# Performance work log

Measured on AMD Instinct MI355X. Metric: run time of the kernel, lower is better.

## Reference

```python
import jax, jax.numpy as jnp
import numpy as np

B, L, V = 128, 32, 10000
IC, WD, H = 2048, 512, 512  # image_code_dim, word_dim, hidden_size (num_layers=1)
D = WD + IC  # GRU input dim


def setup_inputs() -> dict:
    key = jax.random.key(0)
    ks = jax.random.split(key, 10)
    image_code = jax.random.normal(ks[0], (B, IC), dtype=jnp.float32)
    captions = jax.random.randint(ks[1], (B, L), 0, V)
    cap_lens = jax.random.randint(ks[2], (B,), 2, L + 1)
    cap_lens = cap_lens.at[0].set(L)  # pin max length -> static T = L-1
    # parameters (embed/fc match init_weights uniform(-0.1,0.1); GRU/init_state ~ small random)
    embed_w = jax.random.uniform(ks[3], (V, WD), minval=-0.1, maxval=0.1, dtype=jnp.float32)
    W_ih = jax.random.normal(ks[4], (3 * H, D), dtype=jnp.float32) * 0.02
    W_hh = jax.random.normal(ks[5], (3 * H, H), dtype=jnp.float32) * 0.02
    b_ih = jnp.zeros((3 * H,), dtype=jnp.float32)
    b_hh = jnp.zeros((3 * H,), dtype=jnp.float32)
    fc_w = jax.random.uniform(ks[6], (V, H), minval=-0.1, maxval=0.1, dtype=jnp.float32)
    fc_b = jnp.zeros((V,), dtype=jnp.float32)
    init_w = jax.random.normal(ks[7], (H, IC), dtype=jnp.float32) * 0.02  # num_layers*H x IC
    init_b = jnp.zeros((H,), dtype=jnp.float32)
    return {"image_code": image_code, "captions": captions, "cap_lens": cap_lens,
            "embed_w": embed_w, "W_ih": W_ih, "W_hh": W_hh, "b_ih": b_ih, "b_hh": b_hh,
            "fc_w": fc_w, "fc_b": fc_b, "init_w": init_w, "init_b": init_b}


def _gru_decode(image_code, captions_s, lengths, h0, embed_w, W_ih, W_hh, b_ih, b_hh, fc_w, fc_b):
    T = L - 1
    emb = embed_w[captions_s]                      # (B, L, WD)
    xs = jnp.concatenate([
        jnp.broadcast_to(image_code[None], (T, B, IC)),
        jnp.transpose(emb[:, :T, :], (1, 0, 2)),   # (T, B, WD)
    ], axis=-1)                                    # (T, B, D)

    def step(h, x_t):
        gi = x_t @ W_ih.T + b_ih                   # (B, 3H)
        gh = h @ W_hh.T + b_hh                     # (B, 3H)
        i_r, i_z, i_n = jnp.split(gi, 3, axis=-1)
        h_r, h_z, h_n = jnp.split(gh, 3, axis=-1)
        r = jax.nn.sigmoid(i_r + h_r)
        z = jax.nn.sigmoid(i_z + h_z)
        n = jnp.tanh(i_n + r * h_n)
        h_new = (1.0 - z) * n + z * h
        return h_new, h_new

    _, outs = jax.lax.scan(step, h0, xs)           # (T, B, H)
    preds = jnp.einsum('tbh,vh->tbv', outs, fc_w) + fc_b  # dropout is identity in eval
    mask = jnp.arange(T)[:, None] < lengths[None, :]      # (T, B): only active steps
    preds = jnp.where(mask[:, :, None], preds, 0.0)
    return jnp.transpose(preds, (1, 0, 2))         # (B, T, V)


def reference(image_code, captions, cap_lens, embed_w, W_ih, W_hh, b_ih, b_hh, fc_w, fc_b, init_w, init_b):
    order = jnp.argsort(-cap_lens)                 # descending sort like torch.sort(..., True)
    sorted_lens = cap_lens[order]
    captions_s = captions[order]
    image_code_s = image_code[order]
    h0 = image_code_s @ init_w.T + init_b          # (B, H) (num_layers = 1)
    lengths = sorted_lens - 1
    predictions = _gru_decode(image_code_s, captions_s, lengths, h0,
                              embed_w, W_ih, W_hh, b_ih, b_hh, fc_w, fc_b)
    return predictions, captions_s, lengths, order
```

## Files before the change

kernel.cpp:

```cpp
#include <hip/hip_runtime.h>
#include <math.h>

#define B_   128
#define L_   32
#define T_   31
#define V_   10000
#define IC_  2048
#define WD_  512
#define H_   512
#define D_   2560
#define G3_  1536
#define NPAD_ 10112
#define NPROD_ 64
#define NCONS_ 158
#define NTEAM_ 2
#define SU_PFX0 1
#define SU_GI0  17
#define SU_FCW0 389
#define SU_WHH0 2917
#define SU_N    3301

typedef short short8 __attribute__((ext_vector_type(8)));
typedef float f32x4  __attribute__((ext_vector_type(4)));
typedef unsigned short ushort_t;
typedef unsigned long long ull_t;

__device__ __forceinline__ unsigned short f2bf(float f) {
    unsigned int u = __builtin_bit_cast(unsigned int, f);
    unsigned int r = (u + 0x7FFFu + ((u >> 16) & 1u)) >> 16;
    return (unsigned short)r;
}
__device__ __forceinline__ float bf2f(unsigned short h) {
    unsigned int u = ((unsigned int)h) << 16;
    return __builtin_bit_cast(float, u);
}
__device__ __forceinline__ f32x4 mfma16(short8 a, short8 b, f32x4 c) {
    return __builtin_amdgcn_mfma_f32_16x16x32_bf16(a, b, c, 0, 0, 0);
}

#define WS_ORDER  0
#define WS_LEN    512
#define WS_TOK    1024
#define WS_BAR    16896
#define WS_GIIMG  16960
#define WS_WHH    803392
#define WS_GIWEMB 2376256
#define WS_OUTS   14565952
#define WS_FCW    18760256

template<bool F32>
__device__ __forceinline__ uint4 load_cvt(const void* src, size_t off) {
    if constexpr (!F32) {
        return *(const uint4*)((const unsigned short*)src + off);
    } else {
        const float* p = (const float*)src + off;
        const float4 x = *(const float4*)p;
        const float4 y = *(const float4*)(p + 4);
        union { unsigned short u[8]; uint4 v; } r;
        r.u[0]=f2bf(x.x); r.u[1]=f2bf(x.y); r.u[2]=f2bf(x.z); r.u[3]=f2bf(x.w);
        r.u[4]=f2bf(y.x); r.u[5]=f2bf(y.y); r.u[6]=f2bf(y.z); r.u[7]=f2bf(y.w);
        return r.v;
    }
}

__global__ __launch_bounds__(256) void k_setup(
    const int* __restrict__ captions,
    const int* __restrict__ cap_lens,
    const float* __restrict__ fc_w,
    const float* __restrict__ W_hh,
    const float* __restrict__ image_code,
    const float* __restrict__ W_ih,
    const float* __restrict__ b_ih,
    const float* __restrict__ init_w,
    const float* __restrict__ init_b,
    const float* __restrict__ embed_w,
    ushort_t* __restrict__ fcw_bf,
    ushort_t* __restrict__ whh_bf,
    float* __restrict__ gi_img,
    ushort_t* __restrict__ gi_wemb,
    ushort_t* __restrict__ outs,
    int* __restrict__ order,
    int* __restrict__ len_i,
    int* __restrict__ bar,
    float* __restrict__ out_tail)
{
    __shared__ __align__(16) ushort_t As[128 * 32];
    __shared__ __align__(16) ushort_t Bs[128 * 32];
    __shared__ int s_len[B_];
    __shared__ int s_ord[B_];
    const int bid = blockIdx.x;
    const int tid = threadIdx.x;

    if (bid >= SU_FCW0 && bid < SU_WHH0) {
        const int idx = (bid - SU_FCW0) * 256 + tid;
        const int row = idx >> 6;
        const int ch  = idx & 63;
        union { unsigned short u[8]; uint4 v; } r;
        if (row < V_) {
            const float* p = fc_w + (size_t)row * 512 + ch * 8;
            const float4 x = *(const float4*)p;
            const float4 y = *(const float4*)(p + 4);
            r.u[0]=f2bf(x.x); r.u[1]=f2bf(x.y); r.u[2]=f2bf(x.z); r.u[3]=f2bf(x.w);
            r.u[4]=f2bf(y.x); r.u[5]=f2bf(y.y); r.u[6]=f2bf(y.z); r.u[7]=f2bf(y.w);
        } else {
            r.v = make_uint4(0, 0, 0, 0);
        }
        *(uint4*)&fcw_bf[(size_t)row * 512 + ch * 8] = r.v;
        return;
    }
    if (bid >= SU_WHH0) {
        const int idx = (bid - SU_WHH0) * 256 + tid;
        const size_t o = (size_t)idx * 8;
        const int g = (int)(o / (48 * 512));
        const int rem = (int)(o % (48 * 512));
        const int j = rem >> 9;
        const int k = rem & 511;
        const int srow = (j >> 4) * 512 + g * 16 + (j & 15);
        const float* p = W_hh + (size_t)srow * 512 + k;
        const float4 x = *(const float4*)p;
        const float4 y = *(const float4*)(p + 4);
        union { unsigned short u[8]; uint4 v; } r;
        r.u[0]=f2bf(x.x); r.u[1]=f2bf(x.y); r.u[2]=f2bf(x.z); r.u[3]=f2bf(x.w);
        r.u[4]=f2bf(y.x); r.u[5]=f2bf(y.y); r.u[6]=f2bf(y.z); r.u[7]=f2bf(y.w);
        *(uint4*)&whh_bf[o] = r.v;
        return;
    }

    if (tid < B_) s_len[tid] = cap_lens[tid];
    __syncthreads();
    if (tid < B_) {
        const int myl = s_len[tid];
        int rank = 0;
        for (int k = 0; k < B_; ++k) {
            const int lk = s_len[k];
            if (lk > myl || (lk == myl && k < tid)) rank++;
        }
        s_ord[rank] = tid;
    }
    __syncthreads();

    if (bid == 0) {
        if (tid == 0) *bar = 0;
        if (tid < B_) {
            const int o = s_ord[tid];
            order[tid] = o;
            const int ln = s_len[o] - 1;
            len_i[tid] = ln;
            out_tail[B_ * L_ + tid]      = (float)ln;
            out_tail[B_ * L_ + B_ + tid] = (float)o;
        }
        __syncthreads();
        for (int i = tid; i < B_ * L_; i += 256) {
            const int b = i / L_, l = i % L_;
            out_tail[i] = (float)captions[s_ord[b] * L_ + l];
        }
        return;
    }

    const int w = tid >> 6, lane = tid & 63, quad = lane >> 4, lr = lane & 15;
    const int srow = tid >> 2, ch = tid & 3;
    const int wm = (w & 1) * 64, wn = (w >> 1) * 64;

    f32x4 acc[4][4];
    const f32x4 z4 = {0.f, 0.f, 0.f, 0.f};
#pragma unroll
    for (int i = 0; i < 4; ++i)
#pragma unroll
        for (int j = 0; j < 4; ++j) acc[i][j] = z4;

    if (bid >= SU_GI0) {
        const int ti = bid - SU_GI0;
        const int t = ti / 12, nt = ti - t * 12;
        const int n0 = nt * 128;
        const int ar0 = captions[s_ord[srow]      * L_ + t];
        const int ar1 = captions[s_ord[srow + 64] * L_ + t];
        const int br0 = n0 + srow, br1 = n0 + srow + 64;
        const float* Wt = W_ih + IC_;

        uint4 a0 = load_cvt<true>(embed_w, (size_t)ar0 * WD_ + ch * 8);
        uint4 a1 = load_cvt<true>(embed_w, (size_t)ar1 * WD_ + ch * 8);
        uint4 b0 = load_cvt<true>(Wt, (size_t)br0 * D_ + ch * 8);
        uint4 b1 = load_cvt<true>(Wt, (size_t)br1 * D_ + ch * 8);

        for (int k0 = 0; k0 < WD_; k0 += 32) {
            __syncthreads();
            *(uint4*)&As[(srow)      * 32 + ch * 8] = a0;
            *(uint4*)&As[(srow + 64) * 32 + ch * 8] = a1;
            *(uint4*)&Bs[(srow)      * 32 + ch * 8] = b0;
            *(uint4*)&Bs[(srow + 64) * 32 + ch * 8] = b1;
            __syncthreads();
            short8 af[4], bfr[4];
#pragma unroll
            for (int i = 0; i < 4; ++i) af[i]  = *(const short8*)&As[(wm + i * 16 + lr) * 32 + quad * 8];
#pragma unroll
            for (int j = 0; j < 4; ++j) bfr[j] = *(const short8*)&Bs[(wn + j * 16 + lr) * 32 + quad * 8];
            if (k0 + 32 < WD_) {
                a0 = load_cvt<true>(embed_w, (size_t)ar0 * WD_ + k0 + 32 + ch * 8);
                a1 = load_cvt<true>(embed_w, (size_t)ar1 * WD_ + k0 + 32 + ch * 8);
                b0 = load_cvt<true>(Wt, (size_t)br0 * D_ + k0 + 32 + ch * 8);
                b1 = load_cvt<true>(Wt, (size_t)br1 * D_ + k0 + 32 + ch * 8);
            }
#pragma unroll
            for (int i = 0; i < 4; ++i)
#pragma unroll
                for (int j = 0; j < 4; ++j) acc[i][j] = mfma16(af[i], bfr[j], acc[i][j]);
        }

#pragma unroll
        for (int i = 0; i < 4; ++i)
#pragma unroll
            for (int r = 0; r < 4; ++r) {
                const int m = t * 128 + wm + i * 16 + quad * 4 + r;
#pragma unroll
                for (int j = 0; j < 4; ++j) {
                    const int n = n0 + wn + j * 16 + lr;
                    gi_wemb[(size_t)m * G3_ + n] = f2bf(acc[i][j][r]);
                }
            }
        return;
    }

    const int px = bid - SU_PFX0;
    const bool isH0 = px >= 12;
    const float* Bm = isH0 ? init_w : W_ih;
    const int ldb = isH0 ? IC_ : D_;
    const int n0 = isH0 ? (px - 12) * 128 : px * 128;
    const float* bias = isH0 ? init_b : b_ih;

    const int ar0 = s_ord[srow];
    const int ar1 = s_ord[srow + 64];
    const int br0 = n0 + srow, br1 = n0 + srow + 64;

    uint4 a0 = load_cvt<true>(image_code, (size_t)ar0 * IC_ + ch * 8);
    uint4 a1 = load_cvt<true>(image_code, (size_t)ar1 * IC_ + ch * 8);
    uint4 b0 = load_cvt<true>(Bm, (size_t)br0 * ldb + ch * 8);
    uint4 b1 = load_cvt<true>(Bm, (size_t)br1 * ldb + ch * 8);

    for (int k0 = 0; k0 < IC_; k0 += 32) {
        __syncthreads();
        *(uint4*)&As[(srow)      * 32 + ch * 8] = a0;
        *(uint4*)&As[(srow + 64) * 32 + ch * 8] = a1;
        *(uint4*)&Bs[(srow)      * 32 + ch * 8] = b0;
        *(uint4*)&Bs[(srow + 64) * 32 + ch * 8] = b1;
        __syncthreads();
        short8 af[4], bfr[4];
#pragma unroll
        for (int i = 0; i < 4; ++i) af[i]  = *(const short8*)&As[(wm + i * 16 + lr) * 32 + quad * 8];
#pragma unroll
        for (int j = 0; j < 4; ++j) bfr[j] = *(const short8*)&Bs[(wn + j * 16 + lr) * 32 + quad * 8];
        if (k0 + 32 < IC_) {
            a0 = load_cvt<true>(image_code, (size_t)ar0 * IC_ + k0 + 32 + ch * 8);
            a1 = load_cvt<true>(image_code, (size_t)ar1 * IC_ + k0 + 32 + ch * 8);
            b0 = load_cvt<true>(Bm, (size_t)br0 * ldb + k0 + 32 + ch * 8);
            b1 = load_cvt<true>(Bm, (size_t)br1 * ldb + k0 + 32 + ch * 8);
        }
#pragma unroll
        for (int i = 0; i < 4; ++i)
#pragma unroll
            for (int j = 0; j < 4; ++j) acc[i][j] = mfma16(af[i], bfr[j], acc[i][j]);
    }

#pragma unroll
    for (int i = 0; i < 4; ++i)
#pragma unroll
        for (int r = 0; r < 4; ++r) {
            const int m = wm + i * 16 + quad * 4 + r;
#pragma unroll
            for (int j = 0; j < 4; ++j) {
                const int n = n0 + wn + j * 16 + lr;
                const float v = acc[i][j][r] + bias[n];
                if (isH0) outs[(size_t)m * H_ + n] = f2bf(v);
                else      gi_img[(size_t)m * G3_ + n] = v;
            }
        }
}

#define PBS_STR 520
__global__ __launch_bounds__(256, 1) void k_fused(
    const ushort_t* __restrict__ whh_bf,
    const ushort_t* __restrict__ gi_wemb,
    const float* __restrict__ b_hh,
    ushort_t* __restrict__ outs,
    const ushort_t* __restrict__ fcw_bf,
    const float* __restrict__ fc_b,
    const int* __restrict__ len_i,
    float* __restrict__ out,
    int* __restrict__ sync,
    const float* __restrict__ gi_img)
{
    __shared__ __align__(16) ushort_t sm[43008];
    const int bid = blockIdx.x;
    const int tid = threadIdx.x;
    const int w = tid >> 6, lane = tid & 63, quad = lane >> 4, lr = lane & 15;

    if (bid < NPROD_) {
        __builtin_amdgcn_s_setprio(1);
        const int g = bid & 31;
        const int ih = bid >> 5;
        const bool leader = (bid == (ih << 5));
        ushort_t* Bs = sm;

        const ushort_t* wsrc = whh_bf + (size_t)g * 48 * 512;
        for (int i = tid; i < 48 * 64; i += 256) {
            const int row = i >> 6, c = i & 63;
            *(uint4*)&Bs[row * PBS_STR + c * 8] = *(const uint4*)&wsrc[row * 512 + c * 8];
        }
        const int cg = g * 16 + lr;
        const float bhr = b_hh[cg];
        const float bhz = b_hh[512 + cg];
        const float bhn = b_hh[1024 + cg];
        __syncthreads();

        float gim0[4], gim1[4], gim2[4];
        float hold_reg[4];
        {
            const ushort_t* h0p = outs + (size_t)ih * 64 * 512;
#pragma unroll
            for (int r = 0; r < 4; ++r) {
                const int b = ih * 64 + w * 16 + quad * 4 + r;
                const float* pim = gi_img + (size_t)b * G3_ + cg;
                gim0[r] = pim[0]; gim1[r] = pim[512]; gim2[r] = pim[1024];
                hold_reg[r] = bf2f(h0p[(size_t)(w * 16 + quad * 4 + r) * 512 + cg]);
            }
        }
        ushort_t gi0[4], gi1[4], gi2[4];
#pragma unroll
        for (int r = 0; r < 4; ++r) {
            const int b = ih * 64 + w * 16 + quad * 4 + r;
            const ushort_t* p = gi_wemb + (size_t)b * G3_ + cg;
            gi0[r] = p[0]; gi1[r] = p[512]; gi2[r] = p[1024];
        }

        for (int step = 0; step < T_; ++step) {
            const ushort_t* hsrc = outs + (size_t)step * (128 * 512) + (size_t)ih * 64 * 512;

            uint4 hv[16];
            const ushort_t* hrow = hsrc + (size_t)(w * 16 + lr) * 512 + quad * 8;
#pragma unroll
            for (int kk = 0; kk < 16; ++kk)
                hv[kk] = *(const uint4*)(hrow + kk * 32);

            f32x4 acc[3];
#pragma unroll
            for (int j = 0; j < 3; ++j) acc[j] = (f32x4){0.f, 0.f, 0.f, 0.f};
#pragma unroll
            for (int kk = 0; kk < 16; ++kk) {
                union { uint4 v; short8 s; } cc; cc.v = hv[kk];
                const short8 af = cc.s;
#pragma unroll
                for (int j = 0; j < 3; ++j) {
                    const short8 bf = *(const short8*)&Bs[(j * 16 + lr) * PBS_STR + kk * 32 + quad * 8];
                    acc[j] = mfma16(af, bf, acc[j]);
                }
            }

            ushort_t* hdst = outs + (size_t)(step + 1) * (128 * 512);
#pragma unroll
            for (int r = 0; r < 4; ++r) {
                const int b = ih * 64 + w * 16 + quad * 4 + r;
                const float ir  = bf2f(gi0[r]) + gim0[r] + bhr;
                const float iz  = bf2f(gi1[r]) + gim1[r] + bhz;
                const float in_ = bf2f(gi2[r]) + gim2[r];
                const float hr = acc[0][r];
                const float hz = acc[1][r];
                const float hn = acc[2][r] + bhn;
                const float rg = 1.f / (1.f + __expf(-(ir + hr)));
                const float zg = 1.f / (1.f + __expf(-(iz + hz)));
                const float nn = tanhf(in_ + rg * hn);
                const float hnew = (1.f - zg) * nn + zg * hold_reg[r];
                const unsigned int hb = (unsigned int)f2bf(hnew);
                hold_reg[r] = bf2f((unsigned short)hb);
                const unsigned int pv = (unsigned int)__shfl_xor((int)hb, 1);
                if ((lr & 1) == 0) {
                    const unsigned int word = hb | (pv << 16);
                    __hip_atomic_store((unsigned int*)&hdst[(size_t)b * 512 + cg], word,
                                       __ATOMIC_RELAXED, __HIP_MEMORY_SCOPE_AGENT);
                }
            }

            asm volatile("s_waitcnt vmcnt(0)" ::: "memory");
            __syncthreads();
            const int tgt = step + 1;
            if (tid == 0)
                __hip_atomic_store(&sync[bid * 8], tgt,
                                   __ATOMIC_RELAXED, __HIP_MEMORY_SCOPE_AGENT);

            ushort_t ng0[4], ng1[4], ng2[4];
            if (step + 1 < T_) {
                const size_t gb = (size_t)(step + 1) * 128 * G3_;
#pragma unroll
                for (int r = 0; r < 4; ++r) {
                    const int b = ih * 64 + w * 16 + quad * 4 + r;
                    const ushort_t* p = gi_wemb + gb + (size_t)b * G3_ + cg;
                    ng0[r] = p[0]; ng1[r] = p[512]; ng2[r] = p[1024];
                }
            }
            asm volatile("" ::: "memory");

            if (w == 0 && (step < T_ - 1 || leader)) {
                const int* pf = &sync[(ih * 32 + (lane & 31)) * 8];
                for (;;) {
                    const int v = __hip_atomic_load(pf, __ATOMIC_RELAXED, __HIP_MEMORY_SCOPE_AGENT);
                    if (__all(v >= tgt)) break;
                    __builtin_amdgcn_s_sleep(1);
                }
                if (leader && lane == 0) {
#pragma unroll
                    for (int k = 0; k < 8; ++k)
                        __hip_atomic_store(&sync[768 + k * 16 + ih], tgt,
                                           __ATOMIC_RELAXED, __HIP_MEMORY_SCOPE_AGENT);
                }
            }
            __syncthreads();
            asm volatile("" ::: "memory");

            if (step + 1 < T_) {
#pragma unroll
                for (int r = 0; r < 4; ++r) { gi0[r] = ng0[r]; gi1[r] = ng1[r]; gi2[r] = ng2[r]; }
            }
        }
    } else {
        const int cid = bid - NPROD_;
        const int nb = cid % 79;
        const int team = cid / 79;
        const int n0 = nb * 128;
        ushort_t* As = sm;
        ushort_t* Bs = sm + 4096;
        const int srow = tid >> 2, ch = tid & 3;
        const int wm = (w & 1) * 64, wn = (w >> 1) * 64;
        const ull_t* hready = (const ull_t*)&sync[768 + (cid & 7) * 16];

        float fcb[4];
#pragma unroll
        for (int j = 0; j < 4; ++j) {
            const int n = n0 + wn + j * 16 + lr;
            fcb[j] = (n < V_) ? fc_b[n] : 0.f;
        }

        for (int t = team; t < T_; t += NTEAM_) {
            if (tid == 0) {
                for (;;) {
                    const ull_t hv8 = __hip_atomic_load(hready, __ATOMIC_RELAXED, __HIP_MEMORY_SCOPE_AGENT);
                    const int l0 = (int)(unsigned int)(hv8 & 0xffffffffull);
                    const int l1 = (int)(unsigned int)(hv8 >> 32);
                    if (l0 > t && l1 > t) break;
                    __builtin_amdgcn_s_sleep(16);
                }
            }
            __syncthreads();

            const ushort_t* A = outs + (size_t)(t + 1) * (128 * 512);

            f32x4 acc[4][4];
            const f32x4 z4 = {0.f, 0.f, 0.f, 0.f};
#pragma unroll
            for (int i = 0; i < 4; ++i)
#pragma unroll
                for (int j = 0; j < 4; ++j) acc[i][j] = z4;

            uint4 a0 = *(const uint4*)&A[(size_t)srow * 512 + ch * 8];
            uint4 a1 = *(const uint4*)&A[(size_t)(srow + 64) * 512 + ch * 8];
            uint4 b0 = *(const uint4*)&fcw_bf[(size_t)(n0 + srow)      * 512 + ch * 8];
            uint4 b1 = *(const uint4*)&fcw_bf[(size_t)(n0 + srow + 64) * 512 + ch * 8];

            for (int k0 = 0; k0 < 512; k0 += 32) {
                __syncthreads();
                *(uint4*)&As[(srow)      * 32 + ch * 8] = a0;
                *(uint4*)&As[(srow + 64) * 32 + ch * 8] = a1;
                *(uint4*)&Bs[(srow)      * 32 + ch * 8] = b0;
                *(uint4*)&Bs[(srow + 64) * 32 + ch * 8] = b1;
                __syncthreads();
                short8 af[4], bfr[4];
#pragma unroll
                for (int i = 0; i < 4; ++i) af[i]  = *(const short8*)&As[(wm + i * 16 + lr) * 32 + quad * 8];
#pragma unroll
                for (int j = 0; j < 4; ++j) bfr[j] = *(const short8*)&Bs[(wn + j * 16 + lr) * 32 + quad * 8];
                if (k0 + 32 < 512) {
                    a0 = *(const uint4*)&A[(size_t)srow * 512 + k0 + 32 + ch * 8];
                    a1 = *(const uint4*)&A[(size_t)(srow + 64) * 512 + k0 + 32 + ch * 8];
                    b0 = *(const uint4*)&fcw_bf[(size_t)(n0 + srow)      * 512 + k0 + 32 + ch * 8];
                    b1 = *(const uint4*)&fcw_bf[(size_t)(n0 + srow + 64) * 512 + k0 + 32 + ch * 8];
                }
#pragma unroll
                for (int i = 0; i < 4; ++i)
#pragma unroll
                    for (int j = 0; j < 4; ++j) acc[i][j] = mfma16(af[i], bfr[j], acc[i][j]);
            }

#pragma unroll
            for (int i = 0; i < 4; ++i)
#pragma unroll
                for (int r = 0; r < 4; ++r) {
                    const int b = wm + i * 16 + quad * 4 + r;
                    const bool act = (t < len_i[b]);
                    const size_t base = (size_t)b * T_ * V_ + (size_t)t * V_;
#pragma unroll
                    for (int j = 0; j < 4; ++j) {
                        const int n = n0 + wn + j * 16 + lr;
                        if (n < V_) out[base + n] = act ? (acc[i][j][r] + fcb[j]) : 0.f;
                    }
                }
        }
    }
}

extern "C" void kernel_launch(void* const* d_in, const int* in_sizes, int n_in,
                              void* d_out, int out_size, void* d_ws, size_t ws_size,
                              hipStream_t stream) {
    const float* image_code = (const float*)d_in[0];
    const int*   captions   = (const int*)d_in[1];
    const int*   cap_lens   = (const int*)d_in[2];
    const float* embed_w    = (const float*)d_in[3];
    const float* W_ih       = (const float*)d_in[4];
    const float* W_hh       = (const float*)d_in[5];
    const float* b_ih       = (const float*)d_in[6];
    const float* b_hh       = (const float*)d_in[7];
    const float* fc_w       = (const float*)d_in[8];
    const float* fc_b       = (const float*)d_in[9];
    const float* init_w     = (const float*)d_in[10];
    const float* init_b     = (const float*)d_in[11];

    float* out = (float*)d_out;
    char* ws = (char*)d_ws;
    int*      order   = (int*)(ws + WS_ORDER);
    int*      len_i   = (int*)(ws + WS_LEN);
    int*      bar     = (int*)(ws + WS_BAR);
    float*    gi_img  = (float*)(ws + WS_GIIMG);
    ushort_t* whh_bf  = (ushort_t*)(ws + WS_WHH);
    ushort_t* gi_wemb = (ushort_t*)(ws + WS_GIWEMB);
    ushort_t* outs_bf = (ushort_t*)(ws + WS_OUTS);
    ushort_t* fcw_bf  = (ushort_t*)(ws + WS_FCW);
    int*      sync    = (int*)(fcw_bf + ((size_t)NPAD_ - 4) * 512);

    hipLaunchKernelGGL(k_setup, dim3(SU_N), dim3(256), 0, stream,
                       captions, cap_lens, fc_w, W_hh,
                       image_code, W_ih, b_ih, init_w, init_b, embed_w,
                       fcw_bf, whh_bf, gi_img, gi_wemb, outs_bf,
                       order, len_i, bar,
                       out + (size_t)B_ * T_ * V_);

    hipLaunchKernelGGL(k_fused, dim3(NPROD_ + NCONS_), dim3(256), 0, stream,
                       whh_bf, gi_wemb, b_hh, outs_bf,
                       fcw_bf, fc_b, len_i, out, sync, gi_img);
}
```

Measured before the change: 463.4 us.

## Use 1024-thread blocks with 16 producer blocks covering all batch rows

Producer blocks grow to 1024 threads and each now handles two 16-column slices of W_hh across all 128 batch rows, so there are 16 producers instead of 64. The per-step barrier polls fewer flags, and consumers wait on a single ready counter. Consumer blocks also move to 1024 threads, with each warp computing a 32x32 tile and half the threads staging A while the other half stage B. This is meant to cut cross-block synchronisation latency in the recurrent loop, at the cost of more work per producer block and tighter register and occupancy limits with 1024 threads.

```diff
diff --git a/kernel.cpp b/kernel.cpp
--- a/kernel.cpp
+++ b/kernel.cpp
@@ -11,7 +11,7 @@
 #define D_   2560
 #define G3_  1536
 #define NPAD_ 10112
-#define NPROD_ 64
+#define NPROD_ 16
 #define NCONS_ 158
 #define NTEAM_ 2
 #define SU_PFX0 1
@@ -40,7 +40,6 @@
 
 #define WS_ORDER  0
 #define WS_LEN    512
-#define WS_TOK    1024
 #define WS_BAR    16896
 #define WS_GIIMG  16960
 #define WS_WHH    803392
@@ -276,7 +275,7 @@
 }
 
 #define PBS_STR 520
-__global__ __launch_bounds__(256, 1) void k_fused(
+__global__ __launch_bounds__(1024) void k_fused(
     const ushort_t* __restrict__ whh_bf,
     const ushort_t* __restrict__ gi_wemb,
     const float* __restrict__ b_hh,
@@ -288,76 +287,82 @@
     int* __restrict__ sync,
     const float* __restrict__ gi_img)
 {
-    __shared__ __align__(16) ushort_t sm[43008];
+    __shared__ __align__(16) ushort_t sm[2 * 48 * PBS_STR];
     const int bid = blockIdx.x;
     const int tid = threadIdx.x;
     const int w = tid >> 6, lane = tid & 63, quad = lane >> 4, lr = lane & 15;
 
     if (bid < NPROD_) {
         __builtin_amdgcn_s_setprio(1);
-        const int g = bid & 31;
-        const int ih = bid >> 5;
-        const bool leader = (bid == (ih << 5));
+        const int p = bid;
+        const bool leader = (bid == 0);
+        const int slice_sel = w & 1;
+        const int row_grp = w >> 1;
         ushort_t* Bs = sm;
 
-        const ushort_t* wsrc = whh_bf + (size_t)g * 48 * 512;
-        for (int i = tid; i < 48 * 64; i += 256) {
+        for (int i = tid; i < 2 * 48 * 64; i += 1024) {
             const int row = i >> 6, c = i & 63;
-            *(uint4*)&Bs[row * PBS_STR + c * 8] = *(const uint4*)&wsrc[row * 512 + c * 8];
-        }
+            const int s = row >= 48 ? 1 : 0;
+            const int j = row - s * 48;
+            *(uint4*)&Bs[(s * 48 + j) * PBS_STR + c * 8] =
+                *(const uint4*)&whh_bf[((size_t)(2 * p + s) * 48 + j) * 512 + c * 8];
+        }
+        const int g = 2 * p + slice_sel;
         const int cg = g * 16 + lr;
         const float bhr = b_hh[cg];
         const float bhz = b_hh[512 + cg];
         const float bhn = b_hh[1024 + cg];
+        const ushort_t* Bw = Bs + slice_sel * 48 * PBS_STR;
         __syncthreads();
 
         float gim0[4], gim1[4], gim2[4];
         float hold_reg[4];
-        {
-            const ushort_t* h0p = outs + (size_t)ih * 64 * 512;
+#pragma unroll
+        for (int r = 0; r < 4; ++r) {
+            const int b = row_grp * 16 + quad * 4 + r;
+            const float* pim = gi_img + (size_t)b * G3_ + cg;
+            gim0[r] = pim[0]; gim1[r] = pim[512]; gim2[r] = pim[1024];
+            hold_reg[r] = bf2f(outs[(size_t)b * 512 + cg]);
+        }
+        ushort_t gi0[4], gi1[4], gi2[4];
+#pragma unroll
+        for (int r = 0; r < 4; ++r) {
+            const int b = row_grp * 16 + quad * 4 + r;
+            const ushort_t* pg = gi_wemb + (size_t)b * G3_ + cg;
+            gi0[r] = pg[0]; gi1[r] = pg[512]; gi2[r] = pg[1024];
+        }
+
+        for (int step = 0; step < T_; ++step) {
+            const ushort_t* hsrc = outs + (size_t)step * (128 * 512);
+            const ushort_t* hrow = hsrc + (size_t)(row_grp * 16 + lr) * 512 + quad * 8;
+
+            f32x4 acc[3];
+#pragma unroll
+            for (int j = 0; j < 3; ++j) acc[j] = (f32x4){0.f, 0.f, 0.f, 0.f};
+
+#pragma unroll
+            for (int half = 0; half < 2; ++half) {
+                uint4 hv[8];
+#pragma unroll
+                for (int kk = 0; kk < 8; ++kk)
+                    hv[kk] = *(const uint4*)(hrow + (half * 8 + kk) * 32);
+#pragma unroll
+                for (int kk = 0; kk < 8; ++kk) {
+                    union { uint4 v; short8 s; } cc; cc.v = hv[kk];
+                    const short8 af = cc.s;
+                    const int kc = (half * 8 + kk) * 32;
+#pragma unroll
+                    for (int j = 0; j < 3; ++j) {
+                        const short8 bf = *(const short8*)&Bw[(j * 16 + lr) * PBS_STR + kc + quad * 8];
+                        acc[j] = mfma16(af, bf, acc[j]);
+                    }
+                }
+            }
+
+            ushort_t* hdst = outs + (size_t)(step + 1) * (128 * 512);
 #pragma unroll
             for (int r = 0; r < 4; ++r) {
-                const int b = ih * 64 + w * 16 + quad * 4 + r;
-                const float* pim = gi_img + (size_t)b * G3_ + cg;
-                gim0[r] = pim[0]; gim1[r] = pim[512]; gim2[r] = pim[1024];
-                hold_reg[r] = bf2f(h0p[(size_t)(w * 16 + quad * 4 + r) * 512 + cg]);
-            }
-        }
-        ushort_t gi0[4], gi1[4], gi2[4];
-#pragma unroll
-        for (int r = 0; r < 4; ++r) {
-            const int b = ih * 64 + w * 16 + quad * 4 + r;
-            const ushort_t* p = gi_wemb + (size_t)b * G3_ + cg;
-            gi0[r] = p[0]; gi1[r] = p[512]; gi2[r] = p[1024];
-        }
-
-        for (int step = 0; step < T_; ++step) {
-            const ushort_t* hsrc = outs + (size_t)step * (128 * 512) + (size_t)ih * 64 * 512;
-
-            uint4 hv[16];
-            const ushort_t* hrow = hsrc + (size_t)(w * 16 + lr) * 512 + quad * 8;
-#pragma unroll
-            for (int kk = 0; kk < 16; ++kk)
-                hv[kk] = *(const uint4*)(hrow + kk * 32);
-
-            f32x4 acc[3];
-#pragma unroll
-            for (int j = 0; j < 3; ++j) acc[j] = (f32x4){0.f, 0.f, 0.f, 0.f};
-#pragma unroll
-            for (int kk = 0; kk < 16; ++kk) {
-                union { uint4 v; short8 s; } cc; cc.v = hv[kk];
-                const short8 af = cc.s;
-#pragma unroll
-                for (int j = 0; j < 3; ++j) {
-                    const short8 bf = *(const short8*)&Bs[(j * 16 + lr) * PBS_STR + kk * 32 + quad * 8];
-                    acc[j] = mfma16(af, bf, acc[j]);
-                }
-            }
-
-            ushort_t* hdst = outs + (size_t)(step + 1) * (128 * 512);
-#pragma unroll
-            for (int r = 0; r < 4; ++r) {
-                const int b = ih * 64 + w * 16 + quad * 4 + r;
+                const int b = row_grp * 16 + quad * 4 + r;
                 const float ir  = bf2f(gi0[r]) + gim0[r] + bhr;
                 const float iz  = bf2f(gi1[r]) + gim1[r] + bhz;
                 const float in_ = bf2f(gi2[r]) + gim2[r];
@@ -390,15 +395,15 @@
                 const size_t gb = (size_t)(step + 1) * 128 * G3_;
 #pragma unroll
                 for (int r = 0; r < 4; ++r) {
-                    const int b = ih * 64 + w * 16 + quad * 4 + r;
-                    const ushort_t* p = gi_wemb + gb + (size_t)b * G3_ + cg;
-                    ng0[r] = p[0]; ng1[r] = p[512]; ng2[r] = p[1024];
+                    const int b = row_grp * 16 + quad * 4 + r;
+                    const ushort_t* pg = gi_wemb + gb + (size_t)b * G3_ + cg;
+                    ng0[r] = pg[0]; ng1[r] = pg[512]; ng2[r] = pg[1024];
                 }
             }
             asm volatile("" ::: "memory");
 
             if (w == 0 && (step < T_ - 1 || leader)) {
-                const int* pf = &sync[(ih * 32 + (lane & 31)) * 8];
+                const int* pf = &sync[(lane & 15) * 8];
                 for (;;) {
                     const int v = __hip_atomic_load(pf, __ATOMIC_RELAXED, __HIP_MEMORY_SCOPE_AGENT);
                     if (__all(v >= tgt)) break;
@@ -407,7 +412,7 @@
                 if (leader && lane == 0) {
 #pragma unroll
                     for (int k = 0; k < 8; ++k)
-                        __hip_atomic_store(&sync[768 + k * 16 + ih], tgt,
+                        __hip_atomic_store(&sync[768 + k * 16], tgt,
                                            __ATOMIC_RELAXED, __HIP_MEMORY_SCOPE_AGENT);
                 }
             }
@@ -425,78 +430,71 @@
         const int team = cid / 79;
         const int n0 = nb * 128;
         ushort_t* As = sm;
-        ushort_t* Bs = sm + 4096;
-        const int srow = tid >> 2, ch = tid & 3;
-        const int wm = (w & 1) * 64, wn = (w >> 1) * 64;
-        const ull_t* hready = (const ull_t*)&sync[768 + (cid & 7) * 16];
-
-        float fcb[4];
-#pragma unroll
-        for (int j = 0; j < 4; ++j) {
-            const int n = n0 + wn + j * 16 + lr;
+        ushort_t* Bs2 = sm + 4096;
+        const bool stageB = tid >= 512;
+        const int st = tid & 511;
+        const int srow = st >> 2, ch = st & 3;
+        const int qr = (w >> 2) * 32, qc = (w & 3) * 32;
+        const int* hready = &sync[768 + (cid & 7) * 16];
+
+        float fcb[2];
+#pragma unroll
+        for (int j = 0; j < 2; ++j) {
+            const int n = n0 + qc + j * 16 + lr;
             fcb[j] = (n < V_) ? fc_b[n] : 0.f;
         }
 
         for (int t = team; t < T_; t += NTEAM_) {
             if (tid == 0) {
-                for (;;) {
-                    const ull_t hv8 = __hip_atomic_load(hready, __ATOMIC_RELAXED, __HIP_MEMORY_SCOPE_AGENT);
-                    const int l0 = (int)(unsigned int)(hv8 & 0xffffffffull);
-                    const int l1 = (int)(unsigned int)(hv8 >> 32);
-                    if (l0 > t && l1 > t) break;
+                while (__hip_atomic_load(hready, __ATOMIC_RELAXED, __HIP_MEMORY_SCOPE_AGENT) <= t)
                     __builtin_amdgcn_s_sleep(16);
-                }
             }
             __syncthreads();
 
             const ushort_t* A = outs + (size_t)(t + 1) * (128 * 512);
 
-            f32x4 acc[4][4];
+            f32x4 acc[2][2];
             const f32x4 z4 = {0.f, 0.f, 0.f, 0.f};
 #pragma unroll
-            for (int i = 0; i < 4; ++i)
-#pragma unroll
-                for (int j = 0; j < 4; ++j) acc[i][j] = z4;
-
-            uint4 a0 = *(const uint4*)&A[(size_t)srow * 512 + ch * 8];
-            uint4 a1 = *(const uint4*)&A[(size_t)(srow + 64) * 512 + ch * 8];
-            uint4 b0 = *(const uint4*)&fcw_bf[(size_t)(n0 + srow)      * 512 + ch * 8];
-            uint4 b1 = *(const uint4*)&fcw_bf[(size_t)(n0 + srow + 64) * 512 + ch * 8];
+            for (int i = 0; i < 2; ++i)
+#pragma unroll
+                for (int j = 0; j < 2; ++j) acc[i][j] = z4;
+
+            uint4 v0 = stageB
+                ? *(const uint4*)&fcw_bf[(size_t)(n0 + srow) * 512 + ch * 8]
+                : *(const uint4*)&A[(size_t)srow * 512 + ch * 8];
 
             for (int k0 = 0; k0 < 512; k0 += 32) {
                 __syncthreads();
-                *(uint4*)&As[(srow)      * 32 + ch * 8] = a0;
-                *(uint4*)&As[(srow + 64) * 32 + ch * 8] = a1;
-                *(uint4*)&Bs[(srow)      * 32 + ch * 8] = b0;
-                *(uint4*)&Bs[(srow + 64) * 32 + ch * 8] = b1;
+                if (stageB) *(uint4*)&Bs2[srow * 32 + ch * 8] = v0;
+                else        *(uint4*)&As[srow * 32 + ch * 8]  = v0;
                 __syncthreads();
-                short8 af[4], bfr[4];
-#pragma unroll
-                for (int i = 0; i < 4; ++i) af[i]  = *(const short8*)&As[(wm + i * 16 + lr) * 32 + quad * 8];
-#pragma unroll
-                for (int j = 0; j < 4; ++j) bfr[j] = *(const short8*)&Bs[(wn + j * 16 + lr) * 32 + quad * 8];
+                short8 af[2], bfr[2];
+#pragma unroll
+                for (int i = 0; i < 2; ++i) af[i]  = *(const short8*)&As[(qr + i * 16 + lr) * 32 + quad * 8];
+#pragma unroll
+                for (int j = 0; j < 2; ++j) bfr[j] = *(const short8*)&Bs2[(qc + j * 16 + lr) * 32 + quad * 8];
                 if (k0 + 32 < 512) {
-                    a0 = *(const uint4*)&A[(size_t)srow * 512 + k0 + 32 + ch * 8];
-                    a1 = *(const uint4*)&A[(size_t)(srow + 64) * 512 + k0 + 32 + ch * 8];
-                    b0 = *(const uint4*)&fcw_bf[(size_t)(n0 + srow)      * 512 + k0 + 32 + ch * 8];
-                    b1 = *(const uint4*)&fcw_bf[(size_t)(n0 + srow + 64) * 512 + k0 + 32 + ch * 8];
-                }
-#pragma unroll
-                for (int i = 0; i < 4; ++i)
-#pragma unroll
-                    for (int j = 0; j < 4; ++j) acc[i][j] = mfma16(af[i], bfr[j], acc[i][j]);
-            }
-
-#pragma unroll
-            for (int i = 0; i < 4; ++i)
+                    v0 = stageB
+                        ? *(const uint4*)&fcw_bf[(size_t)(n0 + srow) * 512 + k0 + 32 + ch * 8]
+                        : *(const uint4*)&A[(size_t)srow * 512 + k0 + 32 + ch * 8];
+                }
+#pragma unroll
+                for (int i = 0; i < 2; ++i)
+#pragma unroll
+                    for (int j = 0; j < 2; ++j) acc[i][j] = mfma16(af[i], bfr[j], acc[i][j]);
+            }
+
+#pragma unroll
+            for (int i = 0; i < 2; ++i)
 #pragma unroll
                 for (int r = 0; r < 4; ++r) {
-                    const int b = wm + i * 16 + quad * 4 + r;
+                    const int b = qr + i * 16 + quad * 4 + r;
                     const bool act = (t < len_i[b]);
                     const size_t base = (size_t)b * T_ * V_ + (size_t)t * V_;
 #pragma unroll
-                    for (int j = 0; j < 4; ++j) {
-                        const int n = n0 + wn + j * 16 + lr;
+                    for (int j = 0; j < 2; ++j) {
+                        const int n = n0 + qc + j * 16 + lr;
                         if (n < V_) out[base + n] = act ? (acc[i][j][r] + fcb[j]) : 0.f;
                     }
                 }
@@ -539,7 +537,7 @@
                        order, len_i, bar,
                        out + (size_t)B_ * T_ * V_);
 
-    hipLaunchKernelGGL(k_fused, dim3(NPROD_ + NCONS_), dim3(256), 0, stream,
+    hipLaunchKernelGGL(k_fused, dim3(NPROD_ + NCONS_), dim3(1024), 0, stream,
                        whh_bf, gi_wemb, b_hh, outs_bf,
                        fcw_bf, fc_b, len_i, out, sync, gi_img);
 }
```

Result: slower. 619.0 us (+33.6%).

## Fold weight bf16 conversion into fused kernel to overlap with recurrence

Applied to the files above, without the earlier changes.

Removes the fc_w and W_hh fp32-to-bf16 conversion blocks from the setup kernel. Producer blocks now convert their W_hh slice directly into LDS. Consumer blocks convert their fc_w tile into the workspace before waiting on the recurrence, so this work overlaps the producers' startup instead of running serially in the setup kernel. The sync flags move to a dedicated workspace region zeroed by setup. Two consumer teams redundantly convert the same tile, which adds duplicate memory traffic.

```diff
diff --git a/kernel.cpp b/kernel.cpp
--- a/kernel.cpp
+++ b/kernel.cpp
@@ -16,9 +16,7 @@
 #define NTEAM_ 2
 #define SU_PFX0 1
 #define SU_GI0  17
-#define SU_FCW0 389
-#define SU_WHH0 2917
-#define SU_N    3301
+#define SU_N    389
 
 typedef short short8 __attribute__((ext_vector_type(8)));
 typedef float f32x4  __attribute__((ext_vector_type(4)));
@@ -40,10 +38,8 @@
 
 #define WS_ORDER  0
 #define WS_LEN    512
-#define WS_TOK    1024
-#define WS_BAR    16896
+#define WS_SYNC   1024
 #define WS_GIIMG  16960
-#define WS_WHH    803392
 #define WS_GIWEMB 2376256
 #define WS_OUTS   14565952
 #define WS_FCW    18760256
@@ -66,22 +62,18 @@
 __global__ __launch_bounds__(256) void k_setup(
     const int* __restrict__ captions,
     const int* __restrict__ cap_lens,
-    const float* __restrict__ fc_w,
-    const float* __restrict__ W_hh,
     const float* __restrict__ image_code,
     const float* __restrict__ W_ih,
     const float* __restrict__ b_ih,
     const float* __restrict__ init_w,
     const float* __restrict__ init_b,
     const float* __restrict__ embed_w,
-    ushort_t* __restrict__ fcw_bf,
-    ushort_t* __restrict__ whh_bf,
     float* __restrict__ gi_img,
     ushort_t* __restrict__ gi_wemb,
     ushort_t* __restrict__ outs,
     int* __restrict__ order,
     int* __restrict__ len_i,
-    int* __restrict__ bar,
+    int* __restrict__ sync,
     float* __restrict__ out_tail)
 {
     __shared__ __align__(16) ushort_t As[128 * 32];
@@ -91,41 +83,6 @@
     const int bid = blockIdx.x;
     const int tid = threadIdx.x;
 
-    if (bid >= SU_FCW0 && bid < SU_WHH0) {
-        const int idx = (bid - SU_FCW0) * 256 + tid;
-        const int row = idx >> 6;
-        const int ch  = idx & 63;
-        union { unsigned short u[8]; uint4 v; } r;
-        if (row < V_) {
-            const float* p = fc_w + (size_t)row * 512 + ch * 8;
-            const float4 x = *(const float4*)p;
-            const float4 y = *(const float4*)(p + 4);
-            r.u[0]=f2bf(x.x); r.u[1]=f2bf(x.y); r.u[2]=f2bf(x.z); r.u[3]=f2bf(x.w);
-            r.u[4]=f2bf(y.x); r.u[5]=f2bf(y.y); r.u[6]=f2bf(y.z); r.u[7]=f2bf(y.w);
-        } else {
-            r.v = make_uint4(0, 0, 0, 0);
-        }
-        *(uint4*)&fcw_bf[(size_t)row * 512 + ch * 8] = r.v;
-        return;
-    }
-    if (bid >= SU_WHH0) {
-        const int idx = (bid - SU_WHH0) * 256 + tid;
-        const size_t o = (size_t)idx * 8;
-        const int g = (int)(o / (48 * 512));
-        const int rem = (int)(o % (48 * 512));
-        const int j = rem >> 9;
-        const int k = rem & 511;
-        const int srow = (j >> 4) * 512 + g * 16 + (j & 15);
-        const float* p = W_hh + (size_t)srow * 512 + k;
-        const float4 x = *(const float4*)p;
-        const float4 y = *(const float4*)(p + 4);
-        union { unsigned short u[8]; uint4 v; } r;
-        r.u[0]=f2bf(x.x); r.u[1]=f2bf(x.y); r.u[2]=f2bf(x.z); r.u[3]=f2bf(x.w);
-        r.u[4]=f2bf(y.x); r.u[5]=f2bf(y.y); r.u[6]=f2bf(y.z); r.u[7]=f2bf(y.w);
-        *(uint4*)&whh_bf[o] = r.v;
-        return;
-    }
-
     if (tid < B_) s_len[tid] = cap_lens[tid];
     __syncthreads();
     if (tid < B_) {
@@ -140,7 +97,7 @@
     __syncthreads();
 
     if (bid == 0) {
-        if (tid == 0) *bar = 0;
+        for (int i = tid; i < 1024; i += 256) sync[i] = 0;
         if (tid < B_) {
             const int o = s_ord[tid];
             order[tid] = o;
@@ -277,11 +234,12 @@
 
 #define PBS_STR 520
 __global__ __launch_bounds__(256, 1) void k_fused(
-    const ushort_t* __restrict__ whh_bf,
+    const float* __restrict__ W_hh,
     const ushort_t* __restrict__ gi_wemb,
     const float* __restrict__ b_hh,
     ushort_t* __restrict__ outs,
-    const ushort_t* __restrict__ fcw_bf,
+    ushort_t* __restrict__ fcw_bf,
+    const float* __restrict__ fc_w,
     const float* __restrict__ fc_b,
     const int* __restrict__ len_i,
     float* __restrict__ out,
@@ -300,10 +258,16 @@
         const bool leader = (bid == (ih << 5));
         ushort_t* Bs = sm;
 
-        const ushort_t* wsrc = whh_bf + (size_t)g * 48 * 512;
         for (int i = tid; i < 48 * 64; i += 256) {
-            const int row = i >> 6, c = i & 63;
-            *(uint4*)&Bs[row * PBS_STR + c * 8] = *(const uint4*)&wsrc[row * 512 + c * 8];
+            const int row = i >> 6, c8 = (i & 63) * 8;
+            const int srcrow = (row >> 4) * 512 + g * 16 + (row & 15);
+            const float* p = W_hh + (size_t)srcrow * 512 + c8;
+            const float4 x = *(const float4*)p;
+            const float4 y = *(const float4*)(p + 4);
+            union { unsigned short u[8]; uint4 v; } rr;
+            rr.u[0]=f2bf(x.x); rr.u[1]=f2bf(x.y); rr.u[2]=f2bf(x.z); rr.u[3]=f2bf(x.w);
+            rr.u[4]=f2bf(y.x); rr.u[5]=f2bf(y.y); rr.u[6]=f2bf(y.z); rr.u[7]=f2bf(y.w);
+            *(uint4*)&Bs[row * PBS_STR + c8] = rr.v;
         }
         const int cg = g * 16 + lr;
         const float bhr = b_hh[cg];
@@ -430,6 +394,24 @@
         const int wm = (w & 1) * 64, wn = (w >> 1) * 64;
         const ull_t* hready = (const ull_t*)&sync[768 + (cid & 7) * 16];
 
+        for (int i = tid; i < 128 * 64; i += 256) {
+            const int row = n0 + (i >> 6);
+            const int c8 = (i & 63) * 8;
+            union { unsigned short u[8]; uint4 v; } rr;
+            if (row < V_) {
+                const float* p = fc_w + (size_t)row * 512 + c8;
+                const float4 x = *(const float4*)p;
+                const float4 y = *(const float4*)(p + 4);
+                rr.u[0]=f2bf(x.x); rr.u[1]=f2bf(x.y); rr.u[2]=f2bf(x.z); rr.u[3]=f2bf(x.w);
+                rr.u[4]=f2bf(y.x); rr.u[5]=f2bf(y.y); rr.u[6]=f2bf(y.z); rr.u[7]=f2bf(y.w);
+            } else {
+                rr.v = make_uint4(0, 0, 0, 0);
+            }
+            *(uint4*)&fcw_bf[(size_t)row * 512 + c8] = rr.v;
+        }
+        asm volatile("s_waitcnt vmcnt(0)" ::: "memory");
+        __syncthreads();
+
         float fcb[4];
 #pragma unroll
         for (int j = 0; j < 4; ++j) {
@@ -524,22 +506,20 @@
     char* ws = (char*)d_ws;
     int*      order   = (int*)(ws + WS_ORDER);
     int*      len_i   = (int*)(ws + WS_LEN);
-    int*      bar     = (int*)(ws + WS_BAR);
+    int*      sync    = (int*)(ws + WS_SYNC);
     float*    gi_img  = (float*)(ws + WS_GIIMG);
-    ushort_t* whh_bf  = (ushort_t*)(ws + WS_WHH);
     ushort_t* gi_wemb = (ushort_t*)(ws + WS_GIWEMB);
     ushort_t* outs_bf = (ushort_t*)(ws + WS_OUTS);
     ushort_t* fcw_bf  = (ushort_t*)(ws + WS_FCW);
-    int*      sync    = (int*)(fcw_bf + ((size_t)NPAD_ - 4) * 512);
 
     hipLaunchKernelGGL(k_setup, dim3(SU_N), dim3(256), 0, stream,
-                       captions, cap_lens, fc_w, W_hh,
+                       captions, cap_lens,
                        image_code, W_ih, b_ih, init_w, init_b, embed_w,
-                       fcw_bf, whh_bf, gi_img, gi_wemb, outs_bf,
-                       order, len_i, bar,
+                       gi_img, gi_wemb, outs_bf,
+                       order, len_i, sync,
                        out + (size_t)B_ * T_ * V_);
 
     hipLaunchKernelGGL(k_fused, dim3(NPROD_ + NCONS_), dim3(256), 0, stream,
-                       whh_bf, gi_wemb, b_hh, outs_bf,
-                       fcw_bf, fc_b, len_i, out, sync, gi_img);
-}
+                       W_hh, gi_wemb, b_hh, outs_bf,
+                       fcw_bf, fc_w, fc_b, len_i, out, sync, gi_img);
+}
```

Result: slower. 475.5 us (+2.6%).
